# Performance work log

Hardware: AMD Instinct MI355X
Metric: run time of the kernel (lower is better)

## Reference

```python
import jax, jax.numpy as jnp
import numpy as np
from jax import lax

NUM_GROUP = 512    # G: number of FPS centers
GROUP_SIZE = 32    # M: KNN neighbors per center


def setup_inputs() -> dict:
    key = jax.random.key(0)
    xyz = jax.random.normal(key, (32, 8192, 3), dtype=jnp.float32)  # B N 3
    return {"xyz": xyz}


def _fps(xyz, num_group):
    """Iterative farthest point sampling. xyz: [B,N,3] -> idx [B,G] int32.
    Deterministic start at point 0 (matching pointnet2-style fps)."""
    B, N, _ = xyz.shape

    def step(carry, _):
        dists, last_idx = carry                       # dists: [B,N] running min sq-dist
        last = xyz[jnp.arange(B), last_idx]           # [B,3] most recent center
        d = jnp.sum((xyz - last[:, None, :]) ** 2, axis=-1)  # [B,N]
        dists = jnp.minimum(dists, d)
        nxt = jnp.argmax(dists, axis=-1).astype(jnp.int32)   # farthest point
        return (dists, nxt), nxt

    init_idx = jnp.zeros((B,), jnp.int32)
    init_d = jnp.full((B, N), jnp.inf, xyz.dtype)
    (_, _), idxs = lax.scan(step, (init_d, init_idx), None, length=num_group - 1)
    return jnp.concatenate([init_idx[None, :], idxs], axis=0).T  # [B,G]


def reference(xyz):
    B, N, _ = xyz.shape
    G, M = NUM_GROUP, GROUP_SIZE

    fps_idx = _fps(xyz, G)                              # [B,G] int32
    center = xyz[jnp.arange(B)[:, None], fps_idx]       # [B,G,3]

    # KNN: for each center, k nearest points in xyz (squared euclidean)
    # dist2[b,g,n] = |c|^2 + |x|^2 - 2 c.x   -> [B,G,N]
    x2 = jnp.sum(xyz * xyz, axis=-1)                    # [B,N]
    c2 = jnp.sum(center * center, axis=-1)              # [B,G]
    dist2 = c2[:, :, None] + x2[:, None, :] - 2.0 * jnp.einsum('bgd,bnd->bgn', center, xyz)
    _, idx = lax.top_k(-dist2, M)                       # [B,G,M] nearest-first

    neighborhood = xyz[jnp.arange(B)[:, None, None], idx]   # [B,G,M,3]
    neighborhood = neighborhood - center[:, :, None, :]
    return neighborhood, center, fps_idx
```

## Files before the change

### kernel.cpp

```cpp
#include <hip/hip_runtime.h>
#include <math.h>

#define BATCH  32
#define NPTS   8192
#define NGROUP 512
#define MSIZE  32

#define FPS_THREADS 512
#define DYN_LDS_BYTES (NPTS * 16)

typedef float v2f __attribute__((ext_vector_type(2)));

template<int CTRL>
__device__ __forceinline__ float dpp_max_f32(float x) {
    int o = __builtin_amdgcn_update_dpp(0, __float_as_int(x), CTRL, 0xF, 0xF, true);
    float f = __int_as_float(o);
    return x > f ? x : f;
}
template<int CTRL>
__device__ __forceinline__ unsigned dpp_min_u32_keep(unsigned x) {
    unsigned o = (unsigned)__builtin_amdgcn_update_dpp((int)x, (int)x, CTRL, 0xF, 0xF, false);
    return o < x ? o : x;
}
template<int CTRL>
__device__ __forceinline__ unsigned long long dpp_max_u64(unsigned long long k) {
    int lo2 = __builtin_amdgcn_update_dpp(0, (int)(unsigned)k,        CTRL, 0xF, 0xF, true);
    int hi2 = __builtin_amdgcn_update_dpp(0, (int)(unsigned)(k >> 32), CTRL, 0xF, 0xF, true);
    unsigned long long k2 = (((unsigned long long)(unsigned)hi2) << 32) | (unsigned)lo2;
    return k2 > k ? k2 : k;
}

__global__ __launch_bounds__(FPS_THREADS, 2)
void fps_kernel(const float* __restrict__ xyz,
                float* __restrict__ out_center,
                float* __restrict__ out_fps)
{
#pragma clang fp contract(off)
    extern __shared__ float4 sxyz4[];
    __shared__ unsigned long long wkey[2][8];

    const int b    = blockIdx.x;
    const int t    = threadIdx.x;
    const int lane = t & 63;
    const int wid  = t >> 6;
    const float* bp = xyz + (size_t)b * NPTS * 3;
    const float4* bp4 = reinterpret_cast<const float4*>(bp);

    v2f px2[8], py2[8], pz2[8], dist2[8];
    {
        float f[48];
        #pragma unroll
        for (int q = 0; q < 12; ++q) {
            float4 v = bp4[t * 12 + q];
            f[q*4+0] = v.x; f[q*4+1] = v.y; f[q*4+2] = v.z; f[q*4+3] = v.w;
        }
        #pragma unroll
        for (int k = 0; k < 16; ++k)
            sxyz4[t * 16 + k] = make_float4(f[3*k+0], f[3*k+1], f[3*k+2], 0.0f);
        #pragma unroll
        for (int j = 0; j < 8; ++j) {
            px2[j] = (v2f){f[6*j+0], f[6*j+3]};
            py2[j] = (v2f){f[6*j+1], f[6*j+4]};
            pz2[j] = (v2f){f[6*j+2], f[6*j+5]};
            dist2[j] = (v2f){INFINITY, INFINITY};
        }
    }
    __syncthreads();

    if (t == 0) {
        out_fps[(size_t)b * NGROUP] = 0.0f;
        out_center[(size_t)(b * NGROUP) * 3 + 0] = bp[0];
        out_center[(size_t)(b * NGROUP) * 3 + 1] = bp[1];
        out_center[(size_t)(b * NGROUP) * 3 + 2] = bp[2];
    }

    float lx = sxyz4[0].x, ly = sxyz4[0].y, lz = sxyz4[0].z;
    for (int g = 1; g < NGROUP; ++g) {
        const int p = g & 1;

        #pragma unroll
        for (int j = 0; j < 8; ++j) {
            v2f dx = px2[j] - lx;
            v2f dy = py2[j] - ly;
            v2f dz = pz2[j] - lz;
            v2f t1 = dx * dx;
            v2f t2 = dy * dy;
            v2f t3 = dz * dz;
            v2f s  = t1 + t2;
            v2f d  = s + t3;
            dist2[j] = __builtin_elementwise_min(dist2[j], d);
        }
        v2f mm0 = __builtin_elementwise_max(dist2[0], dist2[1]);
        v2f mm1 = __builtin_elementwise_max(dist2[2], dist2[3]);
        v2f mm2 = __builtin_elementwise_max(dist2[4], dist2[5]);
        v2f mm3 = __builtin_elementwise_max(dist2[6], dist2[7]);
        v2f mma = __builtin_elementwise_max(mm0, mm1);
        v2f mmb = __builtin_elementwise_max(mm2, mm3);
        v2f mmc = __builtin_elementwise_max(mma, mmb);
        float m_t = fmaxf(mmc.x, mmc.y);

        float m = m_t;
        m = dpp_max_f32<0xB1>(m);
        m = dpp_max_f32<0x4E>(m);
        m = dpp_max_f32<0x141>(m);
        m = dpp_max_f32<0x140>(m);
        m = dpp_max_f32<0x142>(m);
        m = dpp_max_f32<0x143>(m);
        float wmax = __int_as_float(__builtin_amdgcn_readlane(__float_as_int(m), 63));

        unsigned long long mask = __ballot(m_t == wmax);
        int l = __ffsll((long long)mask) - 1;

        unsigned lj = 0;
        #pragma unroll
        for (int j = 15; j >= 0; --j) {
            float dj = (j & 1) ? dist2[j >> 1].y : dist2[j >> 1].x;
            lj = (dj == wmax) ? (unsigned)j : lj;
        }
        unsigned idx = ((unsigned)t << 4) | lj;
        unsigned widx = (unsigned)__builtin_amdgcn_readlane((int)idx, l);

        if (lane == 63) {
            wkey[p][wid] =
                (((unsigned long long)__float_as_uint(wmax)) << 32) | (unsigned)~widx;
        }
        __syncthreads();

        unsigned long long kq = wkey[p][lane & 7];
        kq = dpp_max_u64<0xB1>(kq);
        kq = dpp_max_u64<0x4E>(kq);
        kq = dpp_max_u64<0x141>(kq);
        int fi = (int)(~(unsigned)kq);

        float4 wc = sxyz4[fi];
        lx = wc.x; ly = wc.y; lz = wc.z;
        if (t == 0) {
            out_fps[(size_t)b * NGROUP + g] = (float)fi;
            out_center[((size_t)(b * NGROUP + g)) * 3 + 0] = wc.x;
            out_center[((size_t)(b * NGROUP + g)) * 3 + 1] = wc.y;
            out_center[((size_t)(b * NGROUP + g)) * 3 + 2] = wc.z;
        }
    }
}

__global__ __launch_bounds__(256)
void knn_kernel(const float* __restrict__ xyz,
                const float* __restrict__ center,
                float* __restrict__ out_nbhd)
{
    const int lane = threadIdx.x & 63;
    const int gid  = blockIdx.x * 4 + (threadIdx.x >> 6);
    const int b    = gid >> 9;
    const float* bp = xyz + (size_t)b * NPTS * 3;
    const float4* bp4 = reinterpret_cast<const float4*>(bp);

    const float cx = center[(size_t)gid*3+0];
    const float cy = center[(size_t)gid*3+1];
    const float cz = center[(size_t)gid*3+2];

    unsigned kl[4];
    #pragma unroll
    for (int k = 0; k < 4; ++k) kl[k] = 0xFFFFFFFFu;

    #pragma unroll 4
    for (int c = 0; c < 32; ++c) {
        int f4 = c * 192 + lane * 3;
        float4 a  = bp4[f4+0];
        float4 bq = bp4[f4+1];
        float4 cq = bp4[f4+2];
        unsigned p0 = (unsigned)(c * 256 + lane * 4);
        v2f xA = (v2f){a.x,  a.w},  yA = (v2f){a.y,  bq.x}, zA = (v2f){a.z,  bq.y};
        v2f xB = (v2f){bq.z, cq.y}, yB = (v2f){bq.w, cq.z}, zB = (v2f){cq.x, cq.w};
        v2f dxA = xA - cx, dyA = yA - cy, dzA = zA - cz;
        v2f dxB = xB - cx, dyB = yB - cy, dzB = zB - cz;
        v2f dA = dxA*dxA + dyA*dyA + dzA*dzA;
        v2f dB = dxB*dxB + dyB*dyB + dzB*dzB;
        float ds[4] = {dA.x, dA.y, dB.x, dB.y};
        #pragma unroll
        for (int k = 0; k < 4; ++k) {
            unsigned key = (__float_as_uint(ds[k]) & 0xFFFFE000u) | (p0 + k);
            if (key < kl[3]) {
                kl[3] = key;
                #pragma unroll
                for (int q = 3; q > 0; --q) {
                    if (kl[q] < kl[q-1]) {
                        unsigned tk = kl[q]; kl[q] = kl[q-1]; kl[q-1] = tk;
                    }
                }
            }
        }
    }

    int keep = 0;
    #pragma unroll 1
    for (int r = 0; r < MSIZE; ++r) {
        unsigned k = kl[0];
        k = dpp_min_u32_keep<0xB1>(k);
        k = dpp_min_u32_keep<0x4E>(k);
        k = dpp_min_u32_keep<0x141>(k);
        k = dpp_min_u32_keep<0x140>(k);
        k = dpp_min_u32_keep<0x142>(k);
        k = dpp_min_u32_keep<0x143>(k);
        unsigned kmin = (unsigned)__builtin_amdgcn_readlane((int)k, 63);
        if (lane == r) keep = (int)(kmin & 0x1FFFu);
        if (kl[0] == kmin) {
            kl[0] = kl[1]; kl[1] = kl[2]; kl[2] = kl[3];
            kl[3] = 0xFFFFFFFFu;
        }
    }

    if (lane < MSIZE) {
        size_t o = ((size_t)gid * MSIZE + lane) * 3;
        float x = bp[keep*3+0], y = bp[keep*3+1], z = bp[keep*3+2];
        out_nbhd[o+0] = x - cx;
        out_nbhd[o+1] = y - cy;
        out_nbhd[o+2] = z - cz;
    }
}

extern "C" void kernel_launch(void* const* d_in, const int* in_sizes, int n_in,
                              void* d_out, int out_size, void* d_ws, size_t ws_size,
                              hipStream_t stream)
{
    const float* xyz = (const float*)d_in[0];
    float* out        = (float*)d_out;
    float* out_nbhd   = out;
    float* out_center = out + (size_t)BATCH*NGROUP*MSIZE*3;
    float* out_fps    = out_center + (size_t)BATCH*NGROUP*3;

    hipFuncSetAttribute(reinterpret_cast<const void*>(fps_kernel),
                        hipFuncAttributeMaxDynamicSharedMemorySize,
                        DYN_LDS_BYTES);

    fps_kernel<<<dim3(BATCH), dim3(FPS_THREADS), DYN_LDS_BYTES, stream>>>(xyz, out_center, out_fps);
    knn_kernel<<<dim3(BATCH*NGROUP/4), dim3(256), 0, stream>>>(xyz, out_center, out_nbhd);
}
```

Baseline: 587.7 us.

## Process four centers per wave in KNN and transpose FPS LDS layout

The KNN kernel now has each wavefront handle four consecutive centers, reusing each loaded point chunk across four distance and top-4 insertion passes, and the grid shrinks fourfold. This is meant to cut redundant global loads of the point cloud. In FPS, the LDS copy is stored transposed (k*512+t), which should avoid bank conflicts on the initial store. The per-lane argmax index search becomes a min-reduction tree instead of a serial select chain. The cost is more registers per KNN thread and fewer waves in flight.

Result: slower. 601.5 us (+2.3%).

```diff
diff --git a/kernel.cpp b/kernel.cpp
--- a/kernel.cpp
+++ b/kernel.cpp
@@ -56,7 +56,7 @@
         }
         #pragma unroll
         for (int k = 0; k < 16; ++k)
-            sxyz4[t * 16 + k] = make_float4(f[3*k+0], f[3*k+1], f[3*k+2], 0.0f);
+            sxyz4[k * 512 + t] = make_float4(f[3*k+0], f[3*k+1], f[3*k+2], 0.0f);
         #pragma unroll
         for (int j = 0; j < 8; ++j) {
             px2[j] = (v2f){f[6*j+0], f[6*j+3]};
@@ -74,7 +74,7 @@
         out_center[(size_t)(b * NGROUP) * 3 + 2] = bp[2];
     }
 
-    float lx = sxyz4[0].x, ly = sxyz4[0].y, lz = sxyz4[0].z;
+    float lx = bp[0], ly = bp[1], lz = bp[2];
     for (int g = 1; g < NGROUP; ++g) {
         const int p = g & 1;
 
@@ -111,13 +111,18 @@
         unsigned long long mask = __ballot(m_t == wmax);
         int l = __ffsll((long long)mask) - 1;
 
-        unsigned lj = 0;
-        #pragma unroll
-        for (int j = 15; j >= 0; --j) {
+        unsigned cj[16];
+        #pragma unroll
+        for (int j = 0; j < 16; ++j) {
             float dj = (j & 1) ? dist2[j >> 1].y : dist2[j >> 1].x;
-            lj = (dj == wmax) ? (unsigned)j : lj;
-        }
-        unsigned idx = ((unsigned)t << 4) | lj;
+            cj[j] = (dj == wmax) ? (unsigned)j : 16u;
+        }
+        #pragma unroll
+        for (int s = 8; s >= 1; s >>= 1)
+            #pragma unroll
+            for (int i = 0; i < s; ++i)
+                cj[i] = cj[i] < cj[i+s] ? cj[i] : cj[i+s];
+        unsigned idx = ((unsigned)t << 4) | cj[0];
         unsigned widx = (unsigned)__builtin_amdgcn_readlane((int)idx, l);
 
         if (lane == 63) {
@@ -132,7 +137,7 @@
         kq = dpp_max_u64<0x141>(kq);
         int fi = (int)(~(unsigned)kq);
 
-        float4 wc = sxyz4[fi];
+        float4 wc = sxyz4[(fi & 15) * 512 + (fi >> 4)];
         lx = wc.x; ly = wc.y; lz = wc.z;
         if (t == 0) {
             out_fps[(size_t)b * NGROUP + g] = (float)fi;
@@ -149,20 +154,26 @@
                 float* __restrict__ out_nbhd)
 {
     const int lane = threadIdx.x & 63;
-    const int gid  = blockIdx.x * 4 + (threadIdx.x >> 6);
-    const int b    = gid >> 9;
+    const int w    = blockIdx.x * 4 + (threadIdx.x >> 6);
+    const int b    = w >> 7;
+    const int g0   = w * 4;
     const float* bp = xyz + (size_t)b * NPTS * 3;
     const float4* bp4 = reinterpret_cast<const float4*>(bp);
 
-    const float cx = center[(size_t)gid*3+0];
-    const float cy = center[(size_t)gid*3+1];
-    const float cz = center[(size_t)gid*3+2];
-
-    unsigned kl[4];
+    float cx[4], cy[4], cz[4];
     #pragma unroll
-    for (int k = 0; k < 4; ++k) kl[k] = 0xFFFFFFFFu;
-
-    #pragma unroll 4
+    for (int k = 0; k < 4; ++k) {
+        cx[k] = center[(size_t)(g0+k)*3+0];
+        cy[k] = center[(size_t)(g0+k)*3+1];
+        cz[k] = center[(size_t)(g0+k)*3+2];
+    }
+
+    unsigned kl[4][4];
+    #pragma unroll
+    for (int k = 0; k < 4; ++k)
+        #pragma unroll
+        for (int q = 0; q < 4; ++q) kl[k][q] = 0xFFFFFFFFu;
+
     for (int c = 0; c < 32; ++c) {
         int f4 = c * 192 + lane * 3;
         float4 a  = bp4[f4+0];
@@ -171,50 +182,55 @@
         unsigned p0 = (unsigned)(c * 256 + lane * 4);
         v2f xA = (v2f){a.x,  a.w},  yA = (v2f){a.y,  bq.x}, zA = (v2f){a.z,  bq.y};
         v2f xB = (v2f){bq.z, cq.y}, yB = (v2f){bq.w, cq.z}, zB = (v2f){cq.x, cq.w};
-        v2f dxA = xA - cx, dyA = yA - cy, dzA = zA - cz;
-        v2f dxB = xB - cx, dyB = yB - cy, dzB = zB - cz;
-        v2f dA = dxA*dxA + dyA*dyA + dzA*dzA;
-        v2f dB = dxB*dxB + dyB*dyB + dzB*dzB;
-        float ds[4] = {dA.x, dA.y, dB.x, dB.y};
         #pragma unroll
         for (int k = 0; k < 4; ++k) {
-            unsigned key = (__float_as_uint(ds[k]) & 0xFFFFE000u) | (p0 + k);
-            if (key < kl[3]) {
-                kl[3] = key;
-                #pragma unroll
-                for (int q = 3; q > 0; --q) {
-                    if (kl[q] < kl[q-1]) {
-                        unsigned tk = kl[q]; kl[q] = kl[q-1]; kl[q-1] = tk;
+            v2f dxA = xA - cx[k], dyA = yA - cy[k], dzA = zA - cz[k];
+            v2f dxB = xB - cx[k], dyB = yB - cy[k], dzB = zB - cz[k];
+            v2f dA = dxA*dxA + dyA*dyA + dzA*dzA;
+            v2f dB = dxB*dxB + dyB*dyB + dzB*dzB;
+            float ds[4] = {dA.x, dA.y, dB.x, dB.y};
+            #pragma unroll
+            for (int e = 0; e < 4; ++e) {
+                unsigned key = (__float_as_uint(ds[e]) & 0xFFFFE000u) | (p0 + e);
+                if (key < kl[k][3]) {
+                    kl[k][3] = key;
+                    #pragma unroll
+                    for (int q = 3; q > 0; --q) {
+                        if (kl[k][q] < kl[k][q-1]) {
+                            unsigned tk = kl[k][q]; kl[k][q] = kl[k][q-1]; kl[k][q-1] = tk;
+                        }
                     }
                 }
             }
         }
     }
 
-    int keep = 0;
-    #pragma unroll 1
-    for (int r = 0; r < MSIZE; ++r) {
-        unsigned k = kl[0];
-        k = dpp_min_u32_keep<0xB1>(k);
-        k = dpp_min_u32_keep<0x4E>(k);
-        k = dpp_min_u32_keep<0x141>(k);
-        k = dpp_min_u32_keep<0x140>(k);
-        k = dpp_min_u32_keep<0x142>(k);
-        k = dpp_min_u32_keep<0x143>(k);
-        unsigned kmin = (unsigned)__builtin_amdgcn_readlane((int)k, 63);
-        if (lane == r) keep = (int)(kmin & 0x1FFFu);
-        if (kl[0] == kmin) {
-            kl[0] = kl[1]; kl[1] = kl[2]; kl[2] = kl[3];
-            kl[3] = 0xFFFFFFFFu;
-        }
-    }
-
-    if (lane < MSIZE) {
-        size_t o = ((size_t)gid * MSIZE + lane) * 3;
-        float x = bp[keep*3+0], y = bp[keep*3+1], z = bp[keep*3+2];
-        out_nbhd[o+0] = x - cx;
-        out_nbhd[o+1] = y - cy;
-        out_nbhd[o+2] = z - cz;
+    #pragma unroll
+    for (int k = 0; k < 4; ++k) {
+        int keep = 0;
+        #pragma unroll 1
+        for (int r = 0; r < MSIZE; ++r) {
+            unsigned kk = kl[k][0];
+            kk = dpp_min_u32_keep<0xB1>(kk);
+            kk = dpp_min_u32_keep<0x4E>(kk);
+            kk = dpp_min_u32_keep<0x141>(kk);
+            kk = dpp_min_u32_keep<0x140>(kk);
+            kk = dpp_min_u32_keep<0x142>(kk);
+            kk = dpp_min_u32_keep<0x143>(kk);
+            unsigned kmin = (unsigned)__builtin_amdgcn_readlane((int)kk, 63);
+            if (lane == r) keep = (int)(kmin & 0x1FFFu);
+            if (kl[k][0] == kmin) {
+                kl[k][0] = kl[k][1]; kl[k][1] = kl[k][2]; kl[k][2] = kl[k][3];
+                kl[k][3] = 0xFFFFFFFFu;
+            }
+        }
+        if (lane < MSIZE) {
+            size_t o = (((size_t)(g0 + k)) * MSIZE + lane) * 3;
+            float x = bp[keep*3+0], y = bp[keep*3+1], z = bp[keep*3+2];
+            out_nbhd[o+0] = x - cx[k];
+            out_nbhd[o+1] = y - cy[k];
+            out_nbhd[o+2] = z - cz[k];
+        }
     }
 }
 
@@ -233,5 +249,5 @@
                         DYN_LDS_BYTES);
 
     fps_kernel<<<dim3(BATCH), dim3(FPS_THREADS), DYN_LDS_BYTES, stream>>>(xyz, out_center, out_fps);
-    knn_kernel<<<dim3(BATCH*NGROUP/4), dim3(256), 0, stream>>>(xyz, out_center, out_nbhd);
-}
+    knn_kernel<<<dim3(BATCH*NGROUP/16), dim3(256), 0, stream>>>(xyz, out_center, out_nbhd);
+}
```
